# Optimization experiments

Hardware: AMD Instinct MI355X
Metric: run time of the kernel (lower is better)

The kernel has to match this reference:

```python
import jax, jax.numpy as jnp
import numpy as np

N_NODES = 50000
N_EDGES = 800000


def setup_inputs() -> dict:
    key = jax.random.key(0)
    ks = jax.random.split(key, 8)
    x = jax.random.normal(ks[0], (N_NODES, 256), dtype=jnp.float32)
    edge_index = jax.random.randint(ks[1], (2, N_EDGES), 0, N_NODES, dtype=jnp.int64)
    edge_weight = jax.random.uniform(ks[2], (N_EDGES,), dtype=jnp.float32)
    # Glorot-style weights for the 3 GCNConv layers: 256->128->64->32
    def glorot(k, fan_in, fan_out):
        s = jnp.sqrt(6.0 / (fan_in + fan_out))
        return jax.random.uniform(k, (fan_in, fan_out), dtype=jnp.float32, minval=-s, maxval=s)
    return {
        "x": x,
        "edge_index": edge_index,
        "edge_weight": edge_weight,
        "W1": glorot(ks[3], 256, 128), "b1": jnp.zeros((128,), jnp.float32),
        "W2": glorot(ks[4], 128, 64),  "b2": jnp.zeros((64,), jnp.float32),
        "W3": glorot(ks[5], 64, 32),   "b3": jnp.zeros((32,), jnp.float32),
    }


def _gcn_forward(x, row, col, ew, params):
    """Stacked GCNConv+ReLU (PyG semantics: add self loops, symmetric norm)."""
    n = x.shape[0]
    loop = jnp.arange(n, dtype=row.dtype)
    row_f = jnp.concatenate([row, loop])            # [E+N] sources
    col_f = jnp.concatenate([col, loop])            # [E+N] targets
    ew_f = jnp.concatenate([ew, jnp.ones((n,), ew.dtype)])
    deg = jax.ops.segment_sum(ew_f, col_f, num_segments=n)
    dinv = jnp.where(deg > 0, jax.lax.rsqrt(deg), 0.0)
    norm = dinv[row_f] * ew_f * dinv[col_f]         # [E+N]
    for W, b in params:
        h = x @ W                                   # [N, d_out] linear first (PyG order)
        msg = h[row_f] * norm[:, None]              # [E+N, d_out] gather + scale
        agg = jax.ops.segment_sum(msg, col_f, num_segments=n)  # scatter-add
        x = jax.nn.relu(agg + b)                    # fused bias + ReLU
    return x


def reference(x, edge_index, edge_weight, W1, b1, W2, b2, W3, b3):
    row, col = edge_index[0], edge_index[1]
    params = [(W1, b1), (W2, b2), (W3, b3)]
    return _gcn_forward(x, row, col, edge_weight, params)
```

## Files before the change

kernel.cpp:

```cpp
#include <hip/hip_runtime.h>
#include <hip/hip_fp16.h>


#define D0 256
#define D1 128
#define D2 64
#define D3 32

#define NREP 4

#define FIX_SCALE 16777216.0f
#define FIX_INV   (1.0f / 16777216.0f)

typedef _Float16 half8 __attribute__((ext_vector_type(8)));
typedef float floatx4 __attribute__((ext_vector_type(4)));

template <typename SRC>
__device__ __forceinline__ half8 loadA(const SRC* __restrict__ p) {
    if constexpr (sizeof(SRC) == 4) {
        float4 f0 = *(const float4*)p;
        float4 f1 = *(const float4*)(p + 4);
        half8 v;
        v[0] = (_Float16)f0.x; v[1] = (_Float16)f0.y;
        v[2] = (_Float16)f0.z; v[3] = (_Float16)f0.w;
        v[4] = (_Float16)f1.x; v[5] = (_Float16)f1.y;
        v[6] = (_Float16)f1.z; v[7] = (_Float16)f1.w;
        return v;
    } else {
        return *(const half8*)p;
    }
}

template <int K, int BN, typename SRC>
__device__ __forceinline__ void gemm_work(const SRC* __restrict__ X,
                                          const float* __restrict__ W,
                                          _Float16* __restrict__ H, int N,
                                          int w, int totalWaves) {
    constexpr int NC = K / 32;
    constexpr int CG = BN / 32;
    const int lane = threadIdx.x & 63;
    const int quad = lane >> 4;
    const int m = lane & 15;
    const int cg = w & (CG - 1);
    const int nslab = N >> 4;
    const int stride = totalWaves / CG;
    int slab = w / CG;
    if (slab >= nslab) return;
    const int n0 = cg * 32;

    half8 b0[NC], b1[NC];
#pragma unroll
    for (int c = 0; c < NC; ++c) {
#pragma unroll
        for (int j = 0; j < 8; ++j) {
            int k = c * 32 + quad * 8 + j;
            b0[c][j] = (_Float16)W[(size_t)k * BN + n0 + m];
            b1[c][j] = (_Float16)W[(size_t)k * BN + n0 + 16 + m];
        }
    }

    half8 a[NC];
#pragma unroll
    for (int c = 0; c < NC; ++c)
        a[c] = loadA(&X[(size_t)(slab * 16 + m) * K + c * 32 + quad * 8]);

    while (true) {
        const int next = slab + stride;
        half8 an[NC];
        if (next < nslab) {
#pragma unroll
            for (int c = 0; c < NC; ++c)
                an[c] = loadA(&X[(size_t)(next * 16 + m) * K + c * 32 + quad * 8]);
        }

        floatx4 acc0 = (floatx4){0.f, 0.f, 0.f, 0.f};
        floatx4 acc1 = (floatx4){0.f, 0.f, 0.f, 0.f};
#pragma unroll
        for (int c = 0; c < NC; ++c) {
            acc0 = __builtin_amdgcn_mfma_f32_16x16x32_f16(a[c], b0[c], acc0, 0, 0, 0);
            acc1 = __builtin_amdgcn_mfma_f32_16x16x32_f16(a[c], b1[c], acc1, 0, 0, 0);
        }

        const int r0 = slab * 16 + quad * 4;
#pragma unroll
        for (int r = 0; r < 4; ++r) {
            H[(size_t)(r0 + r) * BN + n0 + m]      = (_Float16)acc0[r];
            H[(size_t)(r0 + r) * BN + n0 + 16 + m] = (_Float16)acc1[r];
        }

        if (next >= nslab) break;
        slab = next;
#pragma unroll
        for (int c = 0; c < NC; ++c) a[c] = an[c];
    }
}

__global__ __launch_bounds__(256) void hist_gemm1_kernel(
        const float* __restrict__ x, const float* __restrict__ W1,
        _Float16* __restrict__ h1, int N,
        const int* __restrict__ ei, const float* __restrict__ ew,
        unsigned long long* __restrict__ pk, int* __restrict__ rank, int E,
        int gB) {
    const int b = blockIdx.x;
    if (b < gB) {
        gemm_work<D0, D1, float>(x, W1, h1, N, b * 4 + (threadIdx.x >> 6), gB * 4);
    } else {
        int e = (b - gB) * 256 + threadIdx.x;
        if (e < E) {
            int c = ei[E + e];
            int rep = e & (NREP - 1);
            unsigned int wfix = (unsigned int)(ew[e] * FIX_SCALE + 0.5f);
            unsigned long long old =
                atomicAdd(&pk[(size_t)rep * N + c],
                          (1ULL << 32) | (unsigned long long)wfix);
            rank[e] = (int)(old >> 32);
        }
    }
}

__global__ __launch_bounds__(256) void scan_reduce(const unsigned long long* __restrict__ pk,
                                                   float* __restrict__ dinv,
                                                   int* __restrict__ cnt,
                                                   unsigned* __restrict__ repbase,
                                                   int* __restrict__ blockSum, int N) {
    __shared__ int s[256];
    const int t = threadIdx.x;
    const int i = blockIdx.x * 256 + t;
    int v = 0;
    if (i < N) {
        unsigned long long p0 = pk[i];
        unsigned long long p1 = pk[(size_t)N + i];
        unsigned long long p2 = pk[(size_t)2 * N + i];
        unsigned long long p3 = pk[(size_t)3 * N + i];
        unsigned ws = (unsigned)p0 + (unsigned)p1 + (unsigned)p2 + (unsigned)p3;
        float d = (float)ws * FIX_INV + 1.0f;
        dinv[i] = rsqrtf(d);
        int c0 = (int)(p0 >> 32), c1 = (int)(p1 >> 32);
        int c2 = (int)(p2 >> 32), c3 = (int)(p3 >> 32);
        v = c0 + c1 + c2 + c3;
        cnt[i] = v;
        repbase[i] = (unsigned)c0 | ((unsigned)(c0 + c1) << 8) |
                     ((unsigned)(c0 + c1 + c2) << 16);
    }
    s[t] = v;
    __syncthreads();
#pragma unroll
    for (int off = 128; off > 0; off >>= 1) {
        if (t < off) s[t] += s[t + off];
        __syncthreads();
    }
    if (t == 0) blockSum[blockIdx.x] = s[0];
}

__global__ __launch_bounds__(256) void scan_apply(const int* __restrict__ cnt,
                                                  const int* __restrict__ blockSum,
                                                  int* __restrict__ row_ptr, int N, int B) {
    __shared__ int bs[256];
    __shared__ int s[256];
    const int t = threadIdx.x;
    bs[t] = (t < B) ? blockSum[t] : 0;
    __syncthreads();
#pragma unroll
    for (int off = 1; off < 256; off <<= 1) {
        int u = (t >= off) ? bs[t - off] : 0;
        __syncthreads();
        bs[t] += u;
        __syncthreads();
    }
    const int myOff = (blockIdx.x > 0) ? bs[blockIdx.x - 1] : 0;
    const int i = blockIdx.x * 256 + t;
    const int v = (i < N) ? cnt[i] : 0;
    s[t] = v;
    __syncthreads();
#pragma unroll
    for (int off = 1; off < 256; off <<= 1) {
        int u = (t >= off) ? s[t - off] : 0;
        __syncthreads();
        s[t] += u;
        __syncthreads();
    }
    if (i < N) row_ptr[i] = s[t] - v + myOff;
    if (blockIdx.x == 0 && t == 0) row_ptr[N] = bs[B - 1];
}

__global__ void fill_kernel(const int* __restrict__ ei, const float* __restrict__ ew,
                            const float* __restrict__ dinv,
                            const int* __restrict__ row_ptr, const int* __restrict__ rank,
                            const unsigned* __restrict__ repbase,
                            int2* __restrict__ pairs, int E) {
    int e = blockIdx.x * blockDim.x + threadIdx.x;
    if (e < E) {
        int r = ei[e];
        int c = ei[E + e];
        float w = dinv[r] * ew[e] * dinv[c];
        int rep = e & (NREP - 1);
        unsigned rb = repbase[c];
        int base = rep ? (int)((rb >> ((rep - 1) * 8)) & 0xffu) : 0;
        pairs[row_ptr[c] + base + rank[e]] = make_int2(r, __float_as_int(w));
    }
}

template <int DIN, int DOUT>
__global__ __launch_bounds__(256) void agg_gemm_kernel(
        const _Float16* __restrict__ H, const int* __restrict__ row_ptr,
        const int2* __restrict__ pairs, const float* __restrict__ dinv,
        const float* __restrict__ bias, const float* __restrict__ W,
        _Float16* __restrict__ Hout, int N) {
    constexpr int TPN = DIN / 8;
    constexpr int NPB = 256 / TPN;
    constexpr int NC  = DIN / 32;
    constexpr int S   = NPB / 16;
    constexpr int T   = DOUT / 16;
    static_assert(S * T == 4, "one tile per wave");
    __shared__ _Float16 sA[NPB][DIN + 8];

    const int tid = threadIdx.x;
    const int g = tid / TPN;
    const int sl = tid % TPN;
    const int node0 = blockIdx.x * NPB;
    const int node = node0 + g;
    const bool valid = node < N;

    const int w = tid >> 6;
    const int lane = tid & 63;
    const int q = lane >> 4;
    const int m = lane & 15;
    const int s = w & (S - 1);
    const int t = w / S;
    half8 bf[NC];
#pragma unroll
    for (int c = 0; c < NC; ++c) {
#pragma unroll
        for (int j = 0; j < 8; ++j)
            bf[c][j] = (_Float16)W[(size_t)(c * 32 + q * 8 + j) * DOUT + t * 16 + m];
    }

    float acc[8];
#pragma unroll
    for (int j = 0; j < 8; ++j) acc[j] = 0.0f;

    int beg = 0, end = 0;
    if (valid) { beg = row_ptr[node]; end = row_ptr[node + 1]; }

    if (end > beg) {
        const int last = end - 1;
        int2 p0 = pairs[beg];
        int2 p1 = pairs[min(beg + 1, last)];
        int2 p2 = pairs[min(beg + 2, last)];
        half8 u0 = *(const half8*)&H[(size_t)p0.x * DIN + sl * 8];
        half8 u1 = *(const half8*)&H[(size_t)p1.x * DIN + sl * 8];
        for (int k = beg; k < end; ++k) {
            int2 p3 = pairs[min(k + 3, last)];
            half8 u2 = *(const half8*)&H[(size_t)p2.x * DIN + sl * 8];
            float wv = __int_as_float(p0.y);
#pragma unroll
            for (int j = 0; j < 8; ++j) acc[j] = fmaf(wv, (float)u0[j], acc[j]);
            p0 = p1; p1 = p2; p2 = p3;
            u0 = u1; u1 = u2;
        }
    }

    if (valid) {
        float di = dinv[node];
        float d2 = di * di;
        half8 u = *(const half8*)&H[(size_t)node * DIN + sl * 8];
#pragma unroll
        for (int j = 0; j < 8; ++j) acc[j] = fmaf(d2, (float)u[j], acc[j]);
        float bb[8];
        *(float4*)&bb[0] = *(const float4*)&bias[sl * 8];
        *(float4*)&bb[4] = *(const float4*)&bias[sl * 8 + 4];
        half8 o;
#pragma unroll
        for (int j = 0; j < 8; ++j) o[j] = (_Float16)fmaxf(acc[j] + bb[j], 0.f);
        *(half8*)&sA[g][sl * 8] = o;
    }
    __syncthreads();

    half8 a[NC];
#pragma unroll
    for (int c = 0; c < NC; ++c)
        a[c] = *(const half8*)&sA[s * 16 + m][c * 32 + q * 8];
    floatx4 o4 = (floatx4){0.f, 0.f, 0.f, 0.f};
#pragma unroll
    for (int c = 0; c < NC; ++c)
        o4 = __builtin_amdgcn_mfma_f32_16x16x32_f16(a[c], bf[c], o4, 0, 0, 0);
#pragma unroll
    for (int r = 0; r < 4; ++r) {
        const int nr = node0 + s * 16 + q * 4 + r;
        if (nr < N) Hout[(size_t)nr * DOUT + t * 16 + m] = (_Float16)o4[r];
    }
}

template <int D, typename OUT>
__global__ __launch_bounds__(256) void agg_kernel(const _Float16* __restrict__ H,
                                                  const int* __restrict__ row_ptr,
                                                  const int2* __restrict__ pairs,
                                                  const float* __restrict__ dinv,
                                                  const float* __restrict__ bias,
                                                  OUT* __restrict__ out, int N) {
    constexpr int TPN = D / 8;
    constexpr int NPB = 256 / TPN;
    const int tid = threadIdx.x;
    const int g = tid / TPN;
    const int lane = tid % TPN;
    const int node = blockIdx.x * NPB + g;
    if (node >= N) return;

    const int beg = row_ptr[node];
    const int end = row_ptr[node + 1];
    float acc[8];
#pragma unroll
    for (int j = 0; j < 8; ++j) acc[j] = 0.0f;

    if (end > beg) {
        const int last = end - 1;
        int2 p0 = pairs[beg];
        int2 p1 = pairs[min(beg + 1, last)];
        int2 p2 = pairs[min(beg + 2, last)];
        half8 u0 = *(const half8*)&H[(size_t)p0.x * D + lane * 8];
        half8 u1 = *(const half8*)&H[(size_t)p1.x * D + lane * 8];
        for (int k = beg; k < end; ++k) {
            int2 p3 = pairs[min(k + 3, last)];
            half8 u2 = *(const half8*)&H[(size_t)p2.x * D + lane * 8];
            float w = __int_as_float(p0.y);
#pragma unroll
            for (int j = 0; j < 8; ++j) acc[j] = fmaf(w, (float)u0[j], acc[j]);
            p0 = p1; p1 = p2; p2 = p3;
            u0 = u1; u1 = u2;
        }
    }
    float di = dinv[node];
    float d2 = di * di;
    {
        half8 u = *(const half8*)&H[(size_t)node * D + lane * 8];
#pragma unroll
        for (int j = 0; j < 8; ++j) acc[j] = fmaf(d2, (float)u[j], acc[j]);
    }
    float b[8];
    *(float4*)&b[0] = *(const float4*)&bias[lane * 8];
    *(float4*)&b[4] = *(const float4*)&bias[lane * 8 + 4];
#pragma unroll
    for (int j = 0; j < 8; ++j) acc[j] = fmaxf(acc[j] + b[j], 0.f);

    if constexpr (sizeof(OUT) == 2) {
        half8 o;
#pragma unroll
        for (int j = 0; j < 8; ++j) o[j] = (_Float16)acc[j];
        *(half8*)&out[(size_t)node * D + lane * 8] = o;
    } else {
        float* dst = (float*)&out[(size_t)node * D + lane * 8];
        *(float4*)&dst[0] = make_float4(acc[0], acc[1], acc[2], acc[3]);
        *(float4*)&dst[4] = make_float4(acc[4], acc[5], acc[6], acc[7]);
    }
}

extern "C" void kernel_launch(void* const* d_in, const int* in_sizes, int n_in,
                              void* d_out, int out_size, void* d_ws, size_t ws_size,
                              hipStream_t stream) {
    const float* x   = (const float*)d_in[0];
    const int* ei    = (const int*)d_in[1];
    const float* ew  = (const float*)d_in[2];
    const float* W1  = (const float*)d_in[3];
    const float* b1  = (const float*)d_in[4];
    const float* W2  = (const float*)d_in[5];
    const float* b2  = (const float*)d_in[6];
    const float* W3  = (const float*)d_in[7];
    const float* b3  = (const float*)d_in[8];
    float* out = (float*)d_out;

    const int N = in_sizes[0] / D0;
    const int E = in_sizes[2];
    (void)n_in; (void)out_size; (void)ws_size;

    char* ws = (char*)d_ws;
    size_t off = 0;
    auto carve = [&](size_t bytes) -> void* {
        void* p = (void*)(ws + off);
        off += (bytes + 255) & ~(size_t)255;
        return p;
    };
    unsigned long long* pk = (unsigned long long*)carve((size_t)N * NREP * 8);
    float* dinv    = (float*)carve((size_t)N * 4);
    int*   cnt     = (int*)carve((size_t)N * 4);
    int*   row_ptr = (int*)carve((size_t)(N + 1) * 4);
    int*   rank    = (int*)carve((size_t)E * 4);
    int*   bsum    = (int*)carve(256 * 4);
    unsigned* repbase = (unsigned*)carve((size_t)N * 4);
    int2*  pairs   = (int2*)carve((size_t)E * 8);
    _Float16* bufH = (_Float16*)carve((size_t)N * D1 * 2);
    _Float16* bufO = (_Float16*)carve((size_t)N * D1 * 2);

    _Float16* h1 = bufH;
    _Float16* h2 = bufO;
    _Float16* h3 = bufH;

    const int eb = (E + 255) / 256;
    const int scanB = (N + 255) / 256;
    const int gB = 768;

    hipMemsetAsync(pk, 0, (size_t)N * NREP * 8, stream);
    hist_gemm1_kernel<<<gB + eb, 256, 0, stream>>>(
        x, W1, h1, N, ei, ew, pk, rank, E, gB);

    scan_reduce<<<scanB, 256, 0, stream>>>(pk, dinv, cnt, repbase, bsum, N);
    scan_apply<<<scanB, 256, 0, stream>>>(cnt, bsum, row_ptr, N, scanB);
    fill_kernel<<<eb, 256, 0, stream>>>(ei, ew, dinv, row_ptr, rank, repbase, pairs, E);

    agg_gemm_kernel<D1, D2><<<(N + 15) / 16, 256, 0, stream>>>(
        h1, row_ptr, pairs, dinv, b1, W2, h2, N);

    agg_gemm_kernel<D2, D3><<<(N + 31) / 32, 256, 0, stream>>>(
        h2, row_ptr, pairs, dinv, b2, W3, h3, N);

    agg_kernel<D3, float><<<(N + 63) / 64, 256, 0, stream>>>(
        h3, row_ptr, pairs, dinv, b3, out, N);
}
```

Measured before the change: 259.0 us.

## Build degree histogram in LDS per node-range and edge-slice instead of global atomics

```diff
diff --git a/kernel.cpp b/kernel.cpp
--- a/kernel.cpp
+++ b/kernel.cpp
@@ -7,7 +7,9 @@
 #define D2 64
 #define D3 32
 
-#define NREP 4
+#define NRANGE 8
+#define NSLICE 32
+#define RN_MAX 6256
 
 #define FIX_SCALE 16777216.0f
 #define FIX_INV   (1.0f / 16777216.0f)
@@ -99,57 +101,76 @@
         const float* __restrict__ x, const float* __restrict__ W1,
         _Float16* __restrict__ h1, int N,
         const int* __restrict__ ei, const float* __restrict__ ew,
-        unsigned long long* __restrict__ pk, int* __restrict__ rank, int E,
-        int gB) {
+        unsigned long long* __restrict__ part, int* __restrict__ rank, int E,
+        int hB, int gB) {
+    __shared__ unsigned long long hlds[RN_MAX];
     const int b = blockIdx.x;
-    if (b < gB) {
-        gemm_work<D0, D1, float>(x, W1, h1, N, b * 4 + (threadIdx.x >> 6), gB * 4);
-    } else {
-        int e = (b - gB) * 256 + threadIdx.x;
-        if (e < E) {
-            int c = ei[E + e];
-            int rep = e & (NREP - 1);
-            unsigned int wfix = (unsigned int)(ew[e] * FIX_SCALE + 0.5f);
+    if (b >= hB) {
+        gemm_work<D0, D1, float>(x, W1, h1, N,
+                                 (b - hB) * 4 + (threadIdx.x >> 6), gB * 4);
+        return;
+    }
+    const int t = threadIdx.x;
+    const int r = b & (NRANGE - 1);
+    const int s = b >> 3;
+    const int RNv = (N + NRANGE - 1) / NRANGE;
+    const int r0 = r * RNv;
+    const int rcnt = min(RNv, N - r0);
+
+    for (int i = t; i < rcnt; i += 256) hlds[i] = 0ULL;
+    __syncthreads();
+
+    const int SE = (E + NSLICE - 1) / NSLICE;
+    const int e0 = s * SE;
+    const int e1 = min(e0 + SE, E);
+    for (int e = e0 + t; e < e1; e += 256) {
+        int c = ei[E + e];
+        unsigned rc = (unsigned)(c - r0);
+        if (rc < (unsigned)rcnt) {
+            unsigned wfix = (unsigned)(ew[e] * FIX_SCALE + 0.5f);
             unsigned long long old =
-                atomicAdd(&pk[(size_t)rep * N + c],
-                          (1ULL << 32) | (unsigned long long)wfix);
+                atomicAdd(&hlds[rc], (1ULL << 32) | (unsigned long long)wfix);
             rank[e] = (int)(old >> 32);
         }
     }
-}
-
-__global__ __launch_bounds__(256) void scan_reduce(const unsigned long long* __restrict__ pk,
+    __syncthreads();
+
+    unsigned long long* dst = part + (size_t)s * N + r0;
+    for (int i = t; i < rcnt; i += 256) dst[i] = hlds[i];
+}
+
+__global__ __launch_bounds__(256) void scan_reduce(const unsigned long long* __restrict__ part,
                                                    float* __restrict__ dinv,
                                                    int* __restrict__ cnt,
-                                                   unsigned* __restrict__ repbase,
+                                                   unsigned short* __restrict__ base16,
                                                    int* __restrict__ blockSum, int N) {
-    __shared__ int s[256];
+    __shared__ int sred[256];
     const int t = threadIdx.x;
     const int i = blockIdx.x * 256 + t;
     int v = 0;
     if (i < N) {
-        unsigned long long p0 = pk[i];
-        unsigned long long p1 = pk[(size_t)N + i];
-        unsigned long long p2 = pk[(size_t)2 * N + i];
-        unsigned long long p3 = pk[(size_t)3 * N + i];
-        unsigned ws = (unsigned)p0 + (unsigned)p1 + (unsigned)p2 + (unsigned)p3;
-        float d = (float)ws * FIX_INV + 1.0f;
+        unsigned run = 0;
+        unsigned wsum = 0;
+#pragma unroll
+        for (int s = 0; s < NSLICE; ++s) {
+            unsigned long long p = part[(size_t)s * N + i];
+            base16[(size_t)s * N + i] = (unsigned short)run;
+            run += (unsigned)(p >> 32);
+            wsum += (unsigned)p;
+        }
+        float d = (float)wsum * FIX_INV + 1.0f;
         dinv[i] = rsqrtf(d);
-        int c0 = (int)(p0 >> 32), c1 = (int)(p1 >> 32);
-        int c2 = (int)(p2 >> 32), c3 = (int)(p3 >> 32);
-        v = c0 + c1 + c2 + c3;
+        v = (int)run;
         cnt[i] = v;
-        repbase[i] = (unsigned)c0 | ((unsigned)(c0 + c1) << 8) |
-                     ((unsigned)(c0 + c1 + c2) << 16);
-    }
-    s[t] = v;
+    }
+    sred[t] = v;
     __syncthreads();
 #pragma unroll
     for (int off = 128; off > 0; off >>= 1) {
-        if (t < off) s[t] += s[t + off];
+        if (t < off) sred[t] += sred[t + off];
         __syncthreads();
     }
-    if (t == 0) blockSum[blockIdx.x] = s[0];
+    if (t == 0) blockSum[blockIdx.x] = sred[0];
 }
 
 __global__ __launch_bounds__(256) void scan_apply(const int* __restrict__ cnt,
@@ -186,17 +207,16 @@
 __global__ void fill_kernel(const int* __restrict__ ei, const float* __restrict__ ew,
                             const float* __restrict__ dinv,
                             const int* __restrict__ row_ptr, const int* __restrict__ rank,
-                            const unsigned* __restrict__ repbase,
-                            int2* __restrict__ pairs, int E) {
+                            const unsigned short* __restrict__ base16,
+                            int2* __restrict__ pairs, int E, int N, int SE) {
     int e = blockIdx.x * blockDim.x + threadIdx.x;
     if (e < E) {
         int r = ei[e];
         int c = ei[E + e];
         float w = dinv[r] * ew[e] * dinv[c];
-        int rep = e & (NREP - 1);
-        unsigned rb = repbase[c];
-        int base = rep ? (int)((rb >> ((rep - 1) * 8)) & 0xffu) : 0;
-        pairs[row_ptr[c] + base + rank[e]] = make_int2(r, __float_as_int(w));
+        int s = e / SE;
+        int slot = row_ptr[c] + (int)base16[(size_t)s * N + c] + rank[e];
+        pairs[slot] = make_int2(r, __float_as_int(w));
     }
 }
 
@@ -379,16 +399,19 @@
         off += (bytes + 255) & ~(size_t)255;
         return p;
     };
-    unsigned long long* pk = (unsigned long long*)carve((size_t)N * NREP * 8);
     float* dinv    = (float*)carve((size_t)N * 4);
     int*   cnt     = (int*)carve((size_t)N * 4);
     int*   row_ptr = (int*)carve((size_t)(N + 1) * 4);
     int*   rank    = (int*)carve((size_t)E * 4);
     int*   bsum    = (int*)carve(256 * 4);
-    unsigned* repbase = (unsigned*)carve((size_t)N * 4);
+    unsigned short* base16 = (unsigned short*)carve((size_t)N * NSLICE * 2);
     int2*  pairs   = (int2*)carve((size_t)E * 8);
     _Float16* bufH = (_Float16*)carve((size_t)N * D1 * 2);
-    _Float16* bufO = (_Float16*)carve((size_t)N * D1 * 2);
+    size_t unionBytes = (size_t)N * NSLICE * 8;
+    if ((size_t)N * D1 * 2 > unionBytes) unionBytes = (size_t)N * D1 * 2;
+    char* uni = (char*)carve(unionBytes);
+    unsigned long long* part = (unsigned long long*)uni;
+    _Float16* bufO = (_Float16*)uni;
 
     _Float16* h1 = bufH;
     _Float16* h2 = bufO;
@@ -396,15 +419,16 @@
 
     const int eb = (E + 255) / 256;
     const int scanB = (N + 255) / 256;
-    const int gB = 768;
-
-    hipMemsetAsync(pk, 0, (size_t)N * NREP * 8, stream);
-    hist_gemm1_kernel<<<gB + eb, 256, 0, stream>>>(
-        x, W1, h1, N, ei, ew, pk, rank, E, gB);
-
-    scan_reduce<<<scanB, 256, 0, stream>>>(pk, dinv, cnt, repbase, bsum, N);
+    const int hB = NRANGE * NSLICE;
+    const int gB = 512;
+    const int SE = (E + NSLICE - 1) / NSLICE;
+
+    hist_gemm1_kernel<<<hB + gB, 256, 0, stream>>>(
+        x, W1, h1, N, ei, ew, part, rank, E, hB, gB);
+
+    scan_reduce<<<scanB, 256, 0, stream>>>(part, dinv, cnt, base16, bsum, N);
     scan_apply<<<scanB, 256, 0, stream>>>(cnt, bsum, row_ptr, N, scanB);
-    fill_kernel<<<eb, 256, 0, stream>>>(ei, ew, dinv, row_ptr, rank, repbase, pairs, E);
+    fill_kernel<<<eb, 256, 0, stream>>>(ei, ew, dinv, row_ptr, rank, base16, pairs, E, N, SE);
 
     agg_gemm_kernel<D1, D2><<<(N + 15) / 16, 256, 0, stream>>>(
         h1, row_ptr, pairs, dinv, b1, W2, h2, N);
```

After: 275.8 us. 6.5% more time.

## Drop replicated degree histogram and deepen gather prefetch in aggregation loops

Applied to the files above, without the earlier changes.

```diff
diff --git a/kernel.cpp b/kernel.cpp
--- a/kernel.cpp
+++ b/kernel.cpp
@@ -6,8 +6,6 @@
 #define D1 128
 #define D2 64
 #define D3 32
-
-#define NREP 4
 
 #define FIX_SCALE 16777216.0f
 #define FIX_INV   (1.0f / 16777216.0f)
@@ -108,11 +106,9 @@
         int e = (b - gB) * 256 + threadIdx.x;
         if (e < E) {
             int c = ei[E + e];
-            int rep = e & (NREP - 1);
             unsigned int wfix = (unsigned int)(ew[e] * FIX_SCALE + 0.5f);
             unsigned long long old =
-                atomicAdd(&pk[(size_t)rep * N + c],
-                          (1ULL << 32) | (unsigned long long)wfix);
+                atomicAdd(&pk[c], (1ULL << 32) | (unsigned long long)wfix);
             rank[e] = (int)(old >> 32);
         }
     }
@@ -121,26 +117,17 @@
 __global__ __launch_bounds__(256) void scan_reduce(const unsigned long long* __restrict__ pk,
                                                    float* __restrict__ dinv,
                                                    int* __restrict__ cnt,
-                                                   unsigned* __restrict__ repbase,
                                                    int* __restrict__ blockSum, int N) {
     __shared__ int s[256];
     const int t = threadIdx.x;
     const int i = blockIdx.x * 256 + t;
     int v = 0;
     if (i < N) {
-        unsigned long long p0 = pk[i];
-        unsigned long long p1 = pk[(size_t)N + i];
-        unsigned long long p2 = pk[(size_t)2 * N + i];
-        unsigned long long p3 = pk[(size_t)3 * N + i];
-        unsigned ws = (unsigned)p0 + (unsigned)p1 + (unsigned)p2 + (unsigned)p3;
-        float d = (float)ws * FIX_INV + 1.0f;
+        unsigned long long p = pk[i];
+        float d = (float)(unsigned int)(p & 0xffffffffULL) * FIX_INV + 1.0f;
         dinv[i] = rsqrtf(d);
-        int c0 = (int)(p0 >> 32), c1 = (int)(p1 >> 32);
-        int c2 = (int)(p2 >> 32), c3 = (int)(p3 >> 32);
-        v = c0 + c1 + c2 + c3;
+        v = (int)(p >> 32);
         cnt[i] = v;
-        repbase[i] = (unsigned)c0 | ((unsigned)(c0 + c1) << 8) |
-                     ((unsigned)(c0 + c1 + c2) << 16);
     }
     s[t] = v;
     __syncthreads();
@@ -186,17 +173,13 @@
 __global__ void fill_kernel(const int* __restrict__ ei, const float* __restrict__ ew,
                             const float* __restrict__ dinv,
                             const int* __restrict__ row_ptr, const int* __restrict__ rank,
-                            const unsigned* __restrict__ repbase,
                             int2* __restrict__ pairs, int E) {
     int e = blockIdx.x * blockDim.x + threadIdx.x;
     if (e < E) {
         int r = ei[e];
         int c = ei[E + e];
         float w = dinv[r] * ew[e] * dinv[c];
-        int rep = e & (NREP - 1);
-        unsigned rb = repbase[c];
-        int base = rep ? (int)((rb >> ((rep - 1) * 8)) & 0xffu) : 0;
-        pairs[row_ptr[c] + base + rank[e]] = make_int2(r, __float_as_int(w));
+        pairs[row_ptr[c] + rank[e]] = make_int2(r, __float_as_int(w));
     }
 }
 
@@ -240,35 +223,44 @@
     for (int j = 0; j < 8; ++j) acc[j] = 0.0f;
 
     int beg = 0, end = 0;
-    if (valid) { beg = row_ptr[node]; end = row_ptr[node + 1]; }
+    float di = 0.f;
+    half8 uself = (half8){0,0,0,0,0,0,0,0};
+    float bb[8];
+    if (valid) {
+        beg = row_ptr[node];
+        end = row_ptr[node + 1];
+        di = dinv[node];
+        uself = *(const half8*)&H[(size_t)node * DIN + sl * 8];
+        *(float4*)&bb[0] = *(const float4*)&bias[sl * 8];
+        *(float4*)&bb[4] = *(const float4*)&bias[sl * 8 + 4];
+    }
 
     if (end > beg) {
         const int last = end - 1;
         int2 p0 = pairs[beg];
         int2 p1 = pairs[min(beg + 1, last)];
         int2 p2 = pairs[min(beg + 2, last)];
+        int2 p3 = pairs[min(beg + 3, last)];
+        int2 p4 = pairs[min(beg + 4, last)];
         half8 u0 = *(const half8*)&H[(size_t)p0.x * DIN + sl * 8];
         half8 u1 = *(const half8*)&H[(size_t)p1.x * DIN + sl * 8];
+        half8 u2 = *(const half8*)&H[(size_t)p2.x * DIN + sl * 8];
+        half8 u3 = *(const half8*)&H[(size_t)p3.x * DIN + sl * 8];
         for (int k = beg; k < end; ++k) {
-            int2 p3 = pairs[min(k + 3, last)];
-            half8 u2 = *(const half8*)&H[(size_t)p2.x * DIN + sl * 8];
+            int2 p5 = pairs[min(k + 5, last)];
+            half8 u4 = *(const half8*)&H[(size_t)p4.x * DIN + sl * 8];
             float wv = __int_as_float(p0.y);
 #pragma unroll
             for (int j = 0; j < 8; ++j) acc[j] = fmaf(wv, (float)u0[j], acc[j]);
-            p0 = p1; p1 = p2; p2 = p3;
-            u0 = u1; u1 = u2;
+            p0 = p1; p1 = p2; p2 = p3; p3 = p4; p4 = p5;
+            u0 = u1; u1 = u2; u2 = u3; u3 = u4;
         }
     }
 
     if (valid) {
-        float di = dinv[node];
         float d2 = di * di;
-        half8 u = *(const half8*)&H[(size_t)node * DIN + sl * 8];
-#pragma unroll
-        for (int j = 0; j < 8; ++j) acc[j] = fmaf(d2, (float)u[j], acc[j]);
-        float bb[8];
-        *(float4*)&bb[0] = *(const float4*)&bias[sl * 8];
-        *(float4*)&bb[4] = *(const float4*)&bias[sl * 8 + 4];
+#pragma unroll
+        for (int j = 0; j < 8; ++j) acc[j] = fmaf(d2, (float)uself[j], acc[j]);
         half8 o;
 #pragma unroll
         for (int j = 0; j < 8; ++j) o[j] = (_Float16)fmaxf(acc[j] + bb[j], 0.f);
@@ -308,6 +300,12 @@
 
     const int beg = row_ptr[node];
     const int end = row_ptr[node + 1];
+    const float di = dinv[node];
+    const half8 uself = *(const half8*)&H[(size_t)node * D + lane * 8];
+    float b[8];
+    *(float4*)&b[0] = *(const float4*)&bias[lane * 8];
+    *(float4*)&b[4] = *(const float4*)&bias[lane * 8 + 4];
+
     float acc[8];
 #pragma unroll
     for (int j = 0; j < 8; ++j) acc[j] = 0.0f;
@@ -317,28 +315,25 @@
         int2 p0 = pairs[beg];
         int2 p1 = pairs[min(beg + 1, last)];
         int2 p2 = pairs[min(beg + 2, last)];
+        int2 p3 = pairs[min(beg + 3, last)];
+        int2 p4 = pairs[min(beg + 4, last)];
         half8 u0 = *(const half8*)&H[(size_t)p0.x * D + lane * 8];
         half8 u1 = *(const half8*)&H[(size_t)p1.x * D + lane * 8];
+        half8 u2 = *(const half8*)&H[(size_t)p2.x * D + lane * 8];
+        half8 u3 = *(const half8*)&H[(size_t)p3.x * D + lane * 8];
         for (int k = beg; k < end; ++k) {
-            int2 p3 = pairs[min(k + 3, last)];
-            half8 u2 = *(const half8*)&H[(size_t)p2.x * D + lane * 8];
+            int2 p5 = pairs[min(k + 5, last)];
+            half8 u4 = *(const half8*)&H[(size_t)p4.x * D + lane * 8];
             float w = __int_as_float(p0.y);
 #pragma unroll
             for (int j = 0; j < 8; ++j) acc[j] = fmaf(w, (float)u0[j], acc[j]);
-            p0 = p1; p1 = p2; p2 = p3;
-            u0 = u1; u1 = u2;
-        }
-    }
-    float di = dinv[node];
-    float d2 = di * di;
-    {
-        half8 u = *(const half8*)&H[(size_t)node * D + lane * 8];
-#pragma unroll
-        for (int j = 0; j < 8; ++j) acc[j] = fmaf(d2, (float)u[j], acc[j]);
-    }
-    float b[8];
-    *(float4*)&b[0] = *(const float4*)&bias[lane * 8];
-    *(float4*)&b[4] = *(const float4*)&bias[lane * 8 + 4];
+            p0 = p1; p1 = p2; p2 = p3; p3 = p4; p4 = p5;
+            u0 = u1; u1 = u2; u2 = u3; u3 = u4;
+        }
+    }
+    const float d2 = di * di;
+#pragma unroll
+    for (int j = 0; j < 8; ++j) acc[j] = fmaf(d2, (float)uself[j], acc[j]);
 #pragma unroll
     for (int j = 0; j < 8; ++j) acc[j] = fmaxf(acc[j] + b[j], 0.f);
 
@@ -379,13 +374,12 @@
         off += (bytes + 255) & ~(size_t)255;
         return p;
     };
-    unsigned long long* pk = (unsigned long long*)carve((size_t)N * NREP * 8);
+    unsigned long long* pk = (unsigned long long*)carve((size_t)N * 8);
     float* dinv    = (float*)carve((size_t)N * 4);
     int*   cnt     = (int*)carve((size_t)N * 4);
     int*   row_ptr = (int*)carve((size_t)(N + 1) * 4);
     int*   rank    = (int*)carve((size_t)E * 4);
     int*   bsum    = (int*)carve(256 * 4);
-    unsigned* repbase = (unsigned*)carve((size_t)N * 4);
     int2*  pairs   = (int2*)carve((size_t)E * 8);
     _Float16* bufH = (_Float16*)carve((size_t)N * D1 * 2);
     _Float16* bufO = (_Float16*)carve((size_t)N * D1 * 2);
@@ -398,13 +392,13 @@
     const int scanB = (N + 255) / 256;
     const int gB = 768;
 
-    hipMemsetAsync(pk, 0, (size_t)N * NREP * 8, stream);
+    hipMemsetAsync(pk, 0, (size_t)N * 8, stream);
     hist_gemm1_kernel<<<gB + eb, 256, 0, stream>>>(
         x, W1, h1, N, ei, ew, pk, rank, E, gB);
 
-    scan_reduce<<<scanB, 256, 0, stream>>>(pk, dinv, cnt, repbase, bsum, N);
+    scan_reduce<<<scanB, 256, 0, stream>>>(pk, dinv, cnt, bsum, N);
     scan_apply<<<scanB, 256, 0, stream>>>(cnt, bsum, row_ptr, N, scanB);
-    fill_kernel<<<eb, 256, 0, stream>>>(ei, ew, dinv, row_ptr, rank, repbase, pairs, E);
+    fill_kernel<<<eb, 256, 0, stream>>>(ei, ew, dinv, row_ptr, rank, pairs, E);
 
     agg_gemm_kernel<D1, D2><<<(N + 15) / 16, 256, 0, stream>>>(
         h1, row_ptr, pairs, dinv, b1, W2, h2, N);
```

Measured after the change: 263.0 us. Within noise of the previous version (+1.6%).
